# Kernel optimization log

Hardware: AMD Instinct MI355X
Metric: run time of the kernel (lower is better)

Reference implementation:

```python
import jax, jax.numpy as jnp
import numpy as np

DIM = 768
NUM_HEADS = 12
HEAD_DIM = DIM // NUM_HEADS
SCALE = HEAD_DIM ** (-0.5)
LN_EPS = 1e-5


def setup_inputs() -> dict:
    key = jax.random.key(0)
    ks = jax.random.split(key, 8)
    B, K, C = 4, 2048, DIM
    return {
        "x": jax.random.normal(ks[0], (B, K, C), jnp.float32),
        "pos_embed": jax.random.normal(ks[1], (B, K, C), jnp.float32),
        "rel_pos_bias": jax.random.normal(ks[2], (B, K, K), jnp.float32),
        "ln_g": jnp.ones((C,), jnp.float32),
        "ln_b": jnp.zeros((C,), jnp.float32),
        "qkv_w": jax.random.normal(ks[3], (C, 3 * C), jnp.float32) * 0.02,
        "qkv_b": jnp.zeros((3 * C,), jnp.float32),
        "proj_w": jax.random.normal(ks[4], (C, C), jnp.float32) * 0.02,
        "proj_b": jnp.zeros((C,), jnp.float32),
    }


def _layernorm(x, g, b):
    mu = jnp.mean(x, axis=-1, keepdims=True)
    var = jnp.mean(jnp.square(x - mu), axis=-1, keepdims=True)
    return (x - mu) * jax.lax.rsqrt(var + LN_EPS) * g + b


def reference(x, pos_embed, rel_pos_bias, ln_g, ln_b, qkv_w, qkv_b, proj_w, proj_b):
    B, K, C = x.shape
    H, D = NUM_HEADS, HEAD_DIM
    xp = _layernorm(x, ln_g, ln_b) + pos_embed
    qkv = xp @ qkv_w + qkv_b                      # [B,K,3C]
    qkv = qkv.reshape(B, K, 3, H, D)
    q = jnp.transpose(qkv[:, :, 0], (0, 2, 1, 3))  # [B,H,K,D]
    k = jnp.transpose(qkv[:, :, 1], (0, 2, 1, 3))
    v = jnp.transpose(qkv[:, :, 2], (0, 2, 1, 3))
    attn = jnp.einsum("bhqd,bhkd->bhqk", q, k) * SCALE
    attn = attn + rel_pos_bias[:, None, :, :]
    attn = jax.nn.softmax(attn, axis=-1)
    out = jnp.einsum("bhqk,bhkd->bhqd", attn, v)   # [B,H,K,D]
    out = jnp.transpose(out, (0, 2, 1, 3)).reshape(B, K, C)
    # DropPath(0.1) is identity in eval mode
    return out @ proj_w + proj_b
```

## Files before the change

### kernel.cpp

```cpp
#include <hip/hip_runtime.h>
#include <hip/hip_bf16.h>
#include <stdint.h>

typedef __attribute__((ext_vector_type(4))) float f32x4;
typedef __attribute__((ext_vector_type(16))) float f32x16;
typedef __attribute__((ext_vector_type(8))) short s16x8;
typedef __attribute__((ext_vector_type(4))) short s16x4;
typedef uint16_t u16;

#define DEV __device__ __forceinline__

static DEV u16 f2bf(float f) {
  union { float f; uint32_t u; } v; v.f = f;
  uint32_t r = v.u + 0x7fffu + ((v.u >> 16) & 1u);
  return (u16)(r >> 16);
}

static DEV uint32_t cvt_pk_bf16(float lo, float hi) {
  uint32_t r;
  asm("v_cvt_pk_bf16_f32 %0, %1, %2" : "=v"(r) : "v"(lo), "v"(hi));
  return r;
}

#define GLD_LDS16(gp, lp) __builtin_amdgcn_global_load_lds( \
    (const __attribute__((address_space(1))) void*)(gp),    \
    (__attribute__((address_space(3))) void*)(lp), 16, 0, 0)

__global__ __launch_bounds__(256) void k_ln(
    const float* __restrict__ x, const float* __restrict__ pos,
    const float* __restrict__ g, const float* __restrict__ be,
    u16* __restrict__ xp) {
  int row = blockIdx.x;
  size_t base = (size_t)row * 768;
  int t = threadIdx.x;
  float v0 = x[base + t], v1 = x[base + t + 256], v2 = x[base + t + 512];
  float s = v0 + v1 + v2;
  float ss = v0 * v0 + v1 * v1 + v2 * v2;
#pragma unroll
  for (int off = 1; off < 64; off <<= 1) {
    s += __shfl_xor(s, off);
    ss += __shfl_xor(ss, off);
  }
  __shared__ float red[8];
  int wave = t >> 6, lane = t & 63;
  if (lane == 0) { red[wave] = s; red[4 + wave] = ss; }
  __syncthreads();
  float tot = red[0] + red[1] + red[2] + red[3];
  float tss = red[4] + red[5] + red[6] + red[7];
  float mu = tot * (1.0f / 768.0f);
  float var = tss * (1.0f / 768.0f) - mu * mu;
  float rs = rsqrtf(var + 1e-5f);
  float vv[3] = {v0, v1, v2};
#pragma unroll
  for (int i = 0; i < 3; ++i) {
    int c = t + i * 256;
    float val = (vv[i] - mu) * rs * g[c] + be[c] + pos[base + c];
    xp[base + c] = f2bf(val);
  }
}

__global__ __launch_bounds__(256) void k_tr(
    const float* __restrict__ in, u16* __restrict__ out, int K, int N) {
  __shared__ float tile[32][33];
  int n0 = blockIdx.x * 32, k0 = blockIdx.y * 32;
  int tx = threadIdx.x & 31, ty = threadIdx.x >> 5;
#pragma unroll
  for (int r = ty; r < 32; r += 8)
    tile[r][tx] = in[(size_t)(k0 + r) * N + n0 + tx];
  __syncthreads();
#pragma unroll
  for (int r = ty; r < 32; r += 8)
    out[(size_t)(n0 + r) * K + k0 + tx] = f2bf(tile[tx][r]);
}

__global__ __launch_bounds__(256) void k_gemm_qkv(
    const u16* __restrict__ A, const u16* __restrict__ Bt,
    const float* __restrict__ bias, u16* __restrict__ qkv,
    u16* __restrict__ vtg) {
  __shared__ u16 Al[128 * 64];
  __shared__ u16 Bl[128 * 64];
  const size_t BHKD = (size_t)48 * 2048 * 64;
  int mt = blockIdx.x, nt = blockIdx.y;
  int t = threadIdx.x, wave = t >> 6, lane = t & 63;
  int lr = lane & 15, lg = lane >> 4;
  f32x4 acc[4][4];
#pragma unroll
  for (int i = 0; i < 4; ++i)
#pragma unroll
    for (int j = 0; j < 4; ++j) acc[i][j] = (f32x4){0.f, 0.f, 0.f, 0.f};
  const size_t Ab = (size_t)mt * 128 * 768;
  const size_t Bb = (size_t)nt * 128 * 768;
  int wr = (wave >> 1) * 64, wc = (wave & 1) * 64;
  for (int kt = 0; kt < 12; ++kt) {
#pragma unroll
    for (int c = 0; c < 4; ++c) {
      int q = c * 256 + t;
      int row = q >> 3, ch = q & 7;
      int sc = ch ^ (row & 7);
      GLD_LDS16(A + Ab + (size_t)row * 768 + kt * 64 + sc * 8,
                &Al[(size_t)(c * 256 + wave * 64) * 8]);
      GLD_LDS16(Bt + Bb + (size_t)row * 768 + kt * 64 + sc * 8,
                &Bl[(size_t)(c * 256 + wave * 64) * 8]);
    }
    __syncthreads();
#pragma unroll
    for (int ki = 0; ki < 2; ++ki) {
      s16x8 af[4], bf[4];
#pragma unroll
      for (int mi = 0; mi < 4; ++mi)
        af[mi] = *(const s16x8*)&Al[(wr + mi * 16 + lr) * 64 +
                                    (((ki * 4 + lg) ^ (lr & 7)) * 8)];
#pragma unroll
      for (int ni = 0; ni < 4; ++ni)
        bf[ni] = *(const s16x8*)&Bl[(wc + ni * 16 + lr) * 64 +
                                    (((ki * 4 + lg) ^ (lr & 7)) * 8)];
#pragma unroll
      for (int mi = 0; mi < 4; ++mi)
#pragma unroll
        for (int ni = 0; ni < 4; ++ni)
          acc[mi][ni] = __builtin_amdgcn_mfma_f32_16x16x32_bf16(
              af[mi], bf[ni], acc[mi][ni], 0, 0, 0);
    }
    __syncthreads();
  }
  int which0 = (nt * 128) / 768;
  float qscale = (which0 == 0) ? 0.1803368801f : 1.0f;
#pragma unroll
  for (int ni = 0; ni < 4; ++ni) {
    int col = wc + ni * 16 + lr;
    int n = nt * 128 + col;
    int which = n / 768, cc = n % 768;
    int h = cc >> 6, d = cc & 63;
    float bs = bias[n];
    if (which == 2) {
#pragma unroll
      for (int mi = 0; mi < 4; ++mi) {
        int m0 = mt * 128 + wr + mi * 16 + lg * 4;
        int b = m0 >> 11, kp0 = m0 & 2047;
        s16x4 o4;
#pragma unroll
        for (int j = 0; j < 4; ++j) o4[j] = (short)f2bf(acc[mi][ni][j] + bs);
        *(s16x4*)&vtg[((size_t)(b * 12 + h) * 64 + d) * 2048 + kp0] = o4;
      }
    } else {
#pragma unroll
      for (int mi = 0; mi < 4; ++mi) {
#pragma unroll
        for (int j = 0; j < 4; ++j) {
          int row = wr + mi * 16 + lg * 4 + j;
          int m = mt * 128 + row;
          int b = m >> 11, kp = m & 2047;
          size_t dst = (size_t)which * BHKD +
                       (((size_t)b * 12 + h) * 2048 + kp) * 64 + d;
          qkv[dst] = f2bf((acc[mi][ni][j] + bs) * qscale);
        }
      }
    }
  }
}

#define STAGE_KV(KB, VB, ktt) do {                                          \
  _Pragma("unroll")                                                         \
  for (int c_ = 0; c_ < 2; ++c_) {                                          \
    int q_ = c_ * 256 + t; int r_ = q_ >> 3, ch_ = q_ & 7;                  \
    int sc_ = ch_ ^ (r_ & 7);                                               \
    int gk_ = (r_ & 0x33) | ((r_ & 4) << 1) | ((r_ & 8) >> 1);              \
    GLD_LDS16(Kg + ((size_t)((ktt) * 64 + gk_)) * 64 + sc_ * 8,             \
              &KB[(c_ * 256 + wave * 64) * 8]);                             \
    GLD_LDS16(Vt + (size_t)r_ * 2048 + (ktt) * 64 + sc_ * 8,                \
              &VB[(c_ * 256 + wave * 64) * 8]);                             \
  }                                                                         \
} while (0)

#define LOAD_B(BR, ktt) do {                                                \
  _Pragma("unroll")                                                         \
  for (int kv_ = 0; kv_ < 2; ++kv_) {                                       \
    _Pragma("unroll")                                                       \
    for (int rn_ = 0; rn_ < 2; ++rn_) {                                     \
      const float* bp_ = Bgl + (ktt) * 64 + kv_ * 32 + rn_ * 16;            \
      BR[(kv_ * 2 + rn_) * 2]     = *(const f32x4*)bp_;                     \
      BR[(kv_ * 2 + rn_) * 2 + 1] = *(const f32x4*)(bp_ + 4);               \
    }                                                                       \
  }                                                                         \
} while (0)

#define COMPUTE_TILE(KB, VB, BV) do {                                       \
  f32x16 sa_[2];                                                            \
  _Pragma("unroll")                                                         \
  for (int kv_ = 0; kv_ < 2; ++kv_)                                         \
    _Pragma("unroll")                                                       \
    for (int r = 0; r < 16; ++r)                                            \
      sa_[kv_][r] = 1.4426950409f *                                         \
          BV[kv_ * 4 + (r >> 3) * 2 + ((r >> 2) & 1)][r & 3];               \
  _Pragma("unroll")                                                         \
  for (int ki = 0; ki < 4; ++ki) {                                          \
    _Pragma("unroll")                                                       \
    for (int kv_ = 0; kv_ < 2; ++kv_) {                                     \
      s16x8 kf = *(const s16x8*)&KB[(kv_ * 32 + l31) * 64 +                 \
                                    (((ki * 2 + hi) ^ (l31 & 7)) * 8)];     \
      sa_[kv_] = __builtin_amdgcn_mfma_f32_32x32x16_bf16(kf, qf[ki],        \
                                                         sa_[kv_], 0, 0, 0);\
    }                                                                       \
  }                                                                         \
  float p_[32];                                                             \
  _Pragma("unroll")                                                         \
  for (int kv_ = 0; kv_ < 2; ++kv_)                                         \
    _Pragma("unroll")                                                       \
    for (int r = 0; r < 16; ++r)                                            \
      p_[kv_ * 16 + r] = exp2f(sa_[kv_][r]);                                \
  union { uint32_t u[4]; s16x8 v; } pa_[4];                                 \
  _Pragma("unroll")                                                         \
  for (int s = 0; s < 4; ++s)                                               \
    _Pragma("unroll")                                                       \
    for (int w = 0; w < 4; ++w)                                             \
      pa_[s].u[w] = cvt_pk_bf16(p_[(s >> 1) * 16 + (s & 1) * 8 + 2 * w],    \
                                p_[(s >> 1) * 16 + (s & 1) * 8 + 2 * w + 1]);\
  _Pragma("unroll")                                                         \
  for (int s = 0; s < 4; ++s) {                                             \
    lacc = __builtin_amdgcn_mfma_f32_32x32x16_bf16(onesv, pa_[s].v,         \
                                                   lacc, 0, 0, 0);          \
    _Pragma("unroll")                                                       \
    for (int dt = 0; dt < 2; ++dt) {                                        \
      s16x8 vf = *(const s16x8*)&VB[(dt * 32 + l31) * 64 +                  \
                                    (((s * 2 + hi) ^ (l31 & 7)) * 8)];      \
      oacc[dt] = __builtin_amdgcn_mfma_f32_32x32x16_bf16(vf, pa_[s].v,      \
                                                         oacc[dt], 0, 0, 0);\
    }                                                                       \
  }                                                                         \
} while (0)

__global__ __launch_bounds__(256, 3) void k_attn(
    const u16* __restrict__ qkv, const u16* __restrict__ vtg,
    const float* __restrict__ bias, u16* __restrict__ ctx) {
  __shared__ u16 Kl[3][64 * 64];
  __shared__ u16 Vl[3][64 * 64];
  int bid = blockIdx.x;
  int swz = (bid & 7) * 96 + (bid >> 3);
  int h = swz % 12;
  int bq = swz / 12;
  int qt = bq & 15;
  int b = bq >> 4;
  int bh = b * 12 + h;
  int t = threadIdx.x, wave = t >> 6, lane = t & 63;
  int l31 = lane & 31, hi = lane >> 5;
  const size_t BHKD = (size_t)48 * 2048 * 64;
  const u16* Q = qkv + (size_t)bh * 2048 * 64;
  const u16* Kg = Q + BHKD;
  const u16* Vt = vtg + (size_t)bh * 64 * 2048;
  int qrow = qt * 128 + wave * 32 + l31;
  const float* Bgl = bias + ((size_t)b * 2048 + qrow) * 2048 + hi * 8;
  s16x8 qf[4];
#pragma unroll
  for (int ki = 0; ki < 4; ++ki)
    qf[ki] = *(const s16x8*)&Q[(size_t)qrow * 64 + ki * 16 + hi * 8];
  s16x8 onesv;
#pragma unroll
  for (int i = 0; i < 8; ++i) onesv[i] = (short)0x3F80;
  f32x16 oacc[2], lacc;
#pragma unroll
  for (int r = 0; r < 16; ++r) { oacc[0][r] = 0.f; oacc[1][r] = 0.f; lacc[r] = 0.f; }

  STAGE_KV(Kl[0], Vl[0], 0);
  STAGE_KV(Kl[1], Vl[1], 1);
  asm volatile("s_waitcnt vmcnt(4)" ::: "memory");
  __builtin_amdgcn_s_barrier();
  __builtin_amdgcn_sched_barrier(0);

  int cur = 0;
#pragma unroll 1
  for (int kt = 0; kt < 32; ++kt) {
    f32x4 bv_[8];
    LOAD_B(bv_, kt);
    int nb = cur + 2; if (nb >= 3) nb -= 3;
    if (kt + 2 < 32) STAGE_KV(Kl[nb], Vl[nb], kt + 2);
    COMPUTE_TILE(Kl[cur], Vl[cur], bv_);
    asm volatile("s_waitcnt vmcnt(4)" ::: "memory");
    __builtin_amdgcn_sched_barrier(0);
    __builtin_amdgcn_s_barrier();
    __builtin_amdgcn_sched_barrier(0);
    cur = cur + 1; if (cur >= 3) cur = 0;
  }
  float inv = 1.0f / lacc[0];
  size_t obase = ((size_t)b * 2048 + qrow) * 768 + h * 64;
#pragma unroll
  for (int dt = 0; dt < 2; ++dt) {
#pragma unroll
    for (int g = 0; g < 4; ++g) {
      s16x4 o4;
#pragma unroll
      for (int j = 0; j < 4; ++j)
        o4[j] = (short)f2bf(oacc[dt][g * 4 + j] * inv);
      *(s16x4*)&ctx[obase + dt * 32 + g * 8 + hi * 4] = o4;
    }
  }
}

__global__ __launch_bounds__(256) void k_gemm_proj(
    const u16* __restrict__ A, const u16* __restrict__ Bt,
    const float* __restrict__ bias, float* __restrict__ out) {
  __shared__ u16 Al[128 * 64];
  __shared__ u16 Bl[128 * 64];
  int mt = blockIdx.x, nt = blockIdx.y;
  int t = threadIdx.x, wave = t >> 6, lane = t & 63;
  int lr = lane & 15, lg = lane >> 4;
  f32x4 acc[4][4];
#pragma unroll
  for (int i = 0; i < 4; ++i)
#pragma unroll
    for (int j = 0; j < 4; ++j) acc[i][j] = (f32x4){0.f, 0.f, 0.f, 0.f};
  const size_t Ab = (size_t)mt * 128 * 768;
  const size_t Bb = (size_t)nt * 128 * 768;
  int wr = (wave >> 1) * 64, wc = (wave & 1) * 64;
  for (int kt = 0; kt < 12; ++kt) {
#pragma unroll
    for (int c = 0; c < 4; ++c) {
      int q = c * 256 + t;
      int row = q >> 3, ch = q & 7;
      int sc = ch ^ (row & 7);
      GLD_LDS16(A + Ab + (size_t)row * 768 + kt * 64 + sc * 8,
                &Al[(size_t)(c * 256 + wave * 64) * 8]);
      GLD_LDS16(Bt + Bb + (size_t)row * 768 + kt * 64 + sc * 8,
                &Bl[(size_t)(c * 256 + wave * 64) * 8]);
    }
    __syncthreads();
#pragma unroll
    for (int ki = 0; ki < 2; ++ki) {
      s16x8 af[4], bf[4];
#pragma unroll
      for (int mi = 0; mi < 4; ++mi)
        af[mi] = *(const s16x8*)&Al[(wr + mi * 16 + lr) * 64 +
                                    (((ki * 4 + lg) ^ (lr & 7)) * 8)];
#pragma unroll
      for (int ni = 0; ni < 4; ++ni)
        bf[ni] = *(const s16x8*)&Bl[(wc + ni * 16 + lr) * 64 +
                                    (((ki * 4 + lg) ^ (lr & 7)) * 8)];
#pragma unroll
      for (int mi = 0; mi < 4; ++mi)
#pragma unroll
        for (int ni = 0; ni < 4; ++ni)
          acc[mi][ni] = __builtin_amdgcn_mfma_f32_16x16x32_bf16(
              af[mi], bf[ni], acc[mi][ni], 0, 0, 0);
    }
    __syncthreads();
  }
#pragma unroll
  for (int ni = 0; ni < 4; ++ni) {
    int col = wc + ni * 16 + lr;
    int n = nt * 128 + col;
    float bs = bias[n];
#pragma unroll
    for (int mi = 0; mi < 4; ++mi) {
#pragma unroll
      for (int j = 0; j < 4; ++j) {
        int row = wr + mi * 16 + lg * 4 + j;
        out[(size_t)(mt * 128 + row) * 768 + n] = acc[mi][ni][j] + bs;
      }
    }
  }
}

extern "C" void kernel_launch(void* const* d_in, const int* in_sizes, int n_in,
                              void* d_out, int out_size, void* d_ws, size_t ws_size,
                              hipStream_t stream) {
  const float* x      = (const float*)d_in[0];
  const float* pos    = (const float*)d_in[1];
  const float* bias   = (const float*)d_in[2];
  const float* ln_g   = (const float*)d_in[3];
  const float* ln_b   = (const float*)d_in[4];
  const float* qkv_w  = (const float*)d_in[5];
  const float* qkv_b  = (const float*)d_in[6];
  const float* proj_w = (const float*)d_in[7];
  const float* proj_b = (const float*)d_in[8];
  float* out = (float*)d_out;

  char* ws = (char*)d_ws;
  u16* xp      = (u16*)ws;              ws += 12582912;
  u16* qkv_wt  = (u16*)ws;              ws += 3538944;
  u16* proj_wt = (u16*)ws;              ws += 1179648;
  u16* qkvbuf  = (u16*)ws;              ws += 25165824;
  u16* ctx     = (u16*)ws;              ws += 12582912;
  u16* vtg     = (u16*)ws;              ws += 12582912;

  k_ln<<<8192, 256, 0, stream>>>(x, pos, ln_g, ln_b, xp);
  k_tr<<<dim3(72, 24), 256, 0, stream>>>(qkv_w, qkv_wt, 768, 2304);
  k_tr<<<dim3(24, 24), 256, 0, stream>>>(proj_w, proj_wt, 768, 768);
  k_gemm_qkv<<<dim3(64, 18), 256, 0, stream>>>(xp, qkv_wt, qkv_b, qkvbuf, vtg);
  k_attn<<<768, 256, 0, stream>>>(qkvbuf, vtg, bias, ctx);
  k_gemm_proj<<<dim3(64, 6), 256, 0, stream>>>(ctx, proj_wt, proj_b, out);
}
```

Baseline: 206.8 us.

## Software-pipeline attention loop to overlap next QK with current PV

Splits the per-tile attention compute into a QK part and a PV part. It then software-pipelines the loop with ping-pong score registers, so the QK MFMAs for tile kt+1 are issued alongside the exp and PV MFMAs for tile kt. The loop is unrolled by two with rotating LDS buffer indices, plus a prologue and epilogue. The goal is to hide the latency of the exp and convert steps behind matrix work. In exchange it holds an extra set of accumulator registers, which may pressure occupancy at 3 waves per SIMD. It also replaces the targeted vmcnt waits with plain __syncthreads, which may drain all in-flight prefetches each phase.

```diff
diff --git a/kernel.cpp b/kernel.cpp
--- a/kernel.cpp
+++ b/kernel.cpp
@@ -184,13 +184,12 @@
   }                                                                         \
 } while (0)
 
-#define COMPUTE_TILE(KB, VB, BV) do {                                       \
-  f32x16 sa_[2];                                                            \
+#define QK_PART(SN, KB, BV) do {                                            \
   _Pragma("unroll")                                                         \
   for (int kv_ = 0; kv_ < 2; ++kv_)                                         \
     _Pragma("unroll")                                                       \
     for (int r = 0; r < 16; ++r)                                            \
-      sa_[kv_][r] = 1.4426950409f *                                         \
+      SN[kv_][r] = 1.4426950409f *                                          \
           BV[kv_ * 4 + (r >> 3) * 2 + ((r >> 2) & 1)][r & 3];               \
   _Pragma("unroll")                                                         \
   for (int ki = 0; ki < 4; ++ki) {                                          \
@@ -198,16 +197,19 @@
     for (int kv_ = 0; kv_ < 2; ++kv_) {                                     \
       s16x8 kf = *(const s16x8*)&KB[(kv_ * 32 + l31) * 64 +                 \
                                     (((ki * 2 + hi) ^ (l31 & 7)) * 8)];     \
-      sa_[kv_] = __builtin_amdgcn_mfma_f32_32x32x16_bf16(kf, qf[ki],        \
-                                                         sa_[kv_], 0, 0, 0);\
+      SN[kv_] = __builtin_amdgcn_mfma_f32_32x32x16_bf16(kf, qf[ki],         \
+                                                        SN[kv_], 0, 0, 0);  \
     }                                                                       \
   }                                                                         \
+} while (0)
+
+#define PV_PART(SP, VB) do {                                                \
   float p_[32];                                                             \
   _Pragma("unroll")                                                         \
   for (int kv_ = 0; kv_ < 2; ++kv_)                                         \
     _Pragma("unroll")                                                       \
     for (int r = 0; r < 16; ++r)                                            \
-      p_[kv_ * 16 + r] = exp2f(sa_[kv_][r]);                                \
+      p_[kv_ * 16 + r] = exp2f(SP[kv_][r]);                                 \
   union { uint32_t u[4]; s16x8 v; } pa_[4];                                 \
   _Pragma("unroll")                                                         \
   for (int s = 0; s < 4; ++s)                                               \
@@ -227,6 +229,15 @@
                                                          oacc[dt], 0, 0, 0);\
     }                                                                       \
   }                                                                         \
+} while (0)
+
+#define PHASE(ktt, SP, SN, B0, B1, B2, DOSTAGE, DOQK) do {                  \
+  f32x4 bv_[8];                                                             \
+  if (DOQK) LOAD_B(bv_, (ktt) + 1);                                         \
+  if (DOSTAGE) STAGE_KV(Kl[B2], Vl[B2], (ktt) + 2);                         \
+  if (DOQK) QK_PART(SN, Kl[B1], bv_);                                       \
+  PV_PART(SP, Vl[B0]);                                                      \
+  __syncthreads();                                                          \
 } while (0)
 
 __global__ __launch_bounds__(256, 3) void k_attn(
@@ -259,27 +270,26 @@
   f32x16 oacc[2], lacc;
 #pragma unroll
   for (int r = 0; r < 16; ++r) { oacc[0][r] = 0.f; oacc[1][r] = 0.f; lacc[r] = 0.f; }
+  f32x16 saA[2], saB[2];
 
   STAGE_KV(Kl[0], Vl[0], 0);
   STAGE_KV(Kl[1], Vl[1], 1);
-  asm volatile("s_waitcnt vmcnt(4)" ::: "memory");
-  __builtin_amdgcn_s_barrier();
-  __builtin_amdgcn_sched_barrier(0);
-
-  int cur = 0;
+  {
+    f32x4 bv0[8];
+    LOAD_B(bv0, 0);
+    __syncthreads();
+    QK_PART(saA, Kl[0], bv0);
+  }
+  int c0 = 0, c1 = 1, c2 = 2;
 #pragma unroll 1
-  for (int kt = 0; kt < 32; ++kt) {
-    f32x4 bv_[8];
-    LOAD_B(bv_, kt);
-    int nb = cur + 2; if (nb >= 3) nb -= 3;
-    if (kt + 2 < 32) STAGE_KV(Kl[nb], Vl[nb], kt + 2);
-    COMPUTE_TILE(Kl[cur], Vl[cur], bv_);
-    asm volatile("s_waitcnt vmcnt(4)" ::: "memory");
-    __builtin_amdgcn_sched_barrier(0);
-    __builtin_amdgcn_s_barrier();
-    __builtin_amdgcn_sched_barrier(0);
-    cur = cur + 1; if (cur >= 3) cur = 0;
-  }
+  for (int kt = 0; kt < 30; kt += 2) {
+    PHASE(kt,     saA, saB, c0, c1, c2, 1, 1);
+    PHASE(kt + 1, saB, saA, c1, c2, c0, 1, 1);
+    int tmp = c2; c2 = c1; c1 = c0; c0 = tmp;
+  }
+  PHASE(30, saA, saB, c0, c1, c2, 0, 1);
+  PHASE(31, saB, saA, c1, c2, c0, 0, 0);
+
   float inv = 1.0f / lacc[0];
   size_t obase = ((size_t)b * 2048 + qrow) * 768 + h * 64;
 #pragma unroll
```

New measurement: 263.8 us. +27.6%, slower.
